# Kernel optimization log

Hardware: AMD Instinct MI355X
Metric: run time of the kernel (lower is better)

The kernel has to match this reference:

```python
import jax, jax.numpy as jnp
import numpy as np


def setup_inputs() -> dict:
    key = jax.random.key(0)
    ks = jax.random.split(key, 5)
    B, D, L, E, R = 16384, 1024, 3, 4, 64
    return {
        "x": jax.random.normal(ks[0], (B, D), dtype=jnp.float32),
        "U": jax.random.normal(ks[1], (L, E, D, R), dtype=jnp.float32) * 0.05,
        "V": jax.random.normal(ks[2], (L, E, D, R), dtype=jnp.float32) * 0.05,
        "C": jax.random.normal(ks[3], (L, E, R, R), dtype=jnp.float32) * 0.1,
        "bias": jnp.zeros((L, D), dtype=jnp.float32),
        "G": jax.random.normal(ks[4], (E, D), dtype=jnp.float32) * 0.05,
    }


def reference(x, U, V, C, bias, G):
    # x: (B, D); U,V: (L, E, D, R); C: (L, E, R, R); bias: (L, D); G: (E, D)
    x0 = x
    x_l = x
    n_layers = U.shape[0]
    for i in range(n_layers):
        # low-rank projection per expert: V^T x -> tanh -> C -> tanh -> U
        v = jnp.tanh(jnp.einsum('edr,bd->ber', V[i], x_l))        # (B, E, R)
        c = jnp.tanh(jnp.einsum('ers,bes->ber', C[i], v))          # (B, E, R)
        u = jnp.einsum('edr,ber->bed', U[i], c)                    # (B, E, D)
        expert_out = x0[:, None, :] * (u + bias[i][None, None, :])  # (B, E, D)
        # gating: per-expert Dense(1, no bias) on x_l, softmax over experts
        gate = jax.nn.softmax(jnp.einsum('ed,bd->be', G, x_l), axis=1)  # (B, E)
        x_l = jnp.einsum('bed,be->bd', expert_out, gate) + x_l
    return x_l
```

## Files before the change

### kernel.cpp

```cpp
#include <hip/hip_runtime.h>


typedef __bf16 bf16x8 __attribute__((ext_vector_type(8)));
typedef float f32x4 __attribute__((ext_vector_type(4)));
typedef unsigned short u16;
typedef unsigned int u32;

#define TB   32
#define DIM  1024
#define RR   64
#define NE   4
#define NL   3
#define N1   256

#define VF_PER_LAYER (16*32*2*64*8)
#define UF_PER_LAYER (64*8*2*64*8)
#define VF_TOTAL (NL*VF_PER_LAYER)
#define UF_TOTAL (NL*UF_PER_LAYER)

#define MFMA16(a,b,c) __builtin_amdgcn_mfma_f32_16x16x32_bf16(a,b,c,0,0,0)

__device__ __forceinline__ u16 f2bf(float f) {
  u32 u = __float_as_uint(f);
  u32 r = (u + 0x7FFFu + ((u >> 16) & 1u)) >> 16;
  return (u16)r;
}
__device__ __forceinline__ float bf2f(u16 b) {
  return __uint_as_float(((u32)b) << 16);
}
__device__ __forceinline__ bf16x8 ld_frag_g(const u16* p) {
  return __builtin_bit_cast(bf16x8, *reinterpret_cast<const uint4*>(p));
}

__global__ __launch_bounds__(256)
void convert_frags(const float* __restrict__ Vw, const float* __restrict__ Uw,
                   u16* __restrict__ Vf, u16* __restrict__ Uf) {
  const int id = blockIdx.x * 256 + threadIdx.x;
  float f[8];
  if (id < NL * 16 * 32 * 64) {
    const int lane = id & 63;
    const int ks   = (id >> 6) & 31;
    const int ct   = (id >> 11) & 15;
    const int l    = id >> 15;
    const int col  = ct * 16 + (lane & 15);
    const int e = col >> 6, r = col & 63;
    const int kbase = ks * 32 + (lane >> 4) * 8;
    const float* src = Vw + ((size_t)(l * NE + e) * DIM + kbase) * RR + r;
    #pragma unroll
    for (int i = 0; i < 8; ++i) f[i] = src[(size_t)i * RR];
    u16* dst = Vf + (size_t)l * VF_PER_LAYER + ((((size_t)ct * 32 + ks) * 2) * 64 + lane) * 8;
    uint4 hi, lo;
    u16 h[8], lw[8];
    #pragma unroll
    for (int i = 0; i < 8; ++i) { h[i] = f2bf(f[i]); lw[i] = f2bf(f[i] - bf2f(h[i])); }
    hi.x = h[0] | (u32)h[1] << 16;  hi.y = h[2] | (u32)h[3] << 16;
    hi.z = h[4] | (u32)h[5] << 16;  hi.w = h[6] | (u32)h[7] << 16;
    lo.x = lw[0] | (u32)lw[1] << 16; lo.y = lw[2] | (u32)lw[3] << 16;
    lo.z = lw[4] | (u32)lw[5] << 16; lo.w = lw[6] | (u32)lw[7] << 16;
    *reinterpret_cast<uint4*>(dst) = hi;
    *reinterpret_cast<uint4*>(dst + 512) = lo;
  } else {
    const int u = id - NL * 16 * 32 * 64;
    const int lane = u & 63;
    const int ks   = (u >> 6) & 7;
    const int ct   = (u >> 9) & 63;
    const int l    = u >> 15;
    const int d    = ct * 16 + (lane & 15);
    const int kk   = ks * 32 + (lane >> 4) * 8;
    const int e = kk >> 6, rb = kk & 63;
    const float* src = Uw + ((size_t)(l * NE + e) * DIM + d) * RR + rb;
    #pragma unroll
    for (int i = 0; i < 8; ++i) f[i] = src[i];
    u16* dst = Uf + (size_t)l * UF_PER_LAYER + ((((size_t)ct * 8 + ks) * 2) * 64 + lane) * 8;
    uint4 hi, lo;
    u16 h[8], lw[8];
    #pragma unroll
    for (int i = 0; i < 8; ++i) { h[i] = f2bf(f[i]); lw[i] = f2bf(f[i] - bf2f(h[i])); }
    hi.x = h[0] | (u32)h[1] << 16;  hi.y = h[2] | (u32)h[3] << 16;
    hi.z = h[4] | (u32)h[5] << 16;  hi.w = h[6] | (u32)h[7] << 16;
    lo.x = lw[0] | (u32)lw[1] << 16; lo.y = lw[2] | (u32)lw[3] << 16;
    lo.z = lw[4] | (u32)lw[5] << 16; lo.w = lw[6] | (u32)lw[7] << 16;
    *reinterpret_cast<uint4*>(dst) = hi;
    *reinterpret_cast<uint4*>(dst + 512) = lo;
  }
}

struct SM2 {
  union {
    u16 Ax[2][8][2][64][8];
    u16 Wf[2][8][2][64][8];
  } u;
  float vbuf[TB][N1 + 4];
  float gp[TB][NE][2];
  float gate[TB][NE];
};

__global__ __launch_bounds__(256, 2)
void crossnet_mfma(const float* __restrict__ x,
                   const float* __restrict__ Cw,
                   const float* __restrict__ bias,
                   const float* __restrict__ G,
                   const u16* __restrict__ Vf, const u16* __restrict__ Uf,
                   float* __restrict__ out) {
  __shared__ SM2 sm;
  const int t    = threadIdx.x;
  const int lane = t & 63;
  const int wv   = t >> 6;
  const int l15  = lane & 15;
  const int lg   = lane >> 4;
  const int b0   = blockIdx.x * TB;
  const int tc   = t & 31, tr = t >> 5;

  for (int layer = 0; layer < NL; ++layer) {
    const float* xin = (layer == 0) ? x : out;
    const u16* Vfl = Vf + (size_t)layer * VF_PER_LAYER;
    const u16* Ufl = Uf + (size_t)layer * UF_PER_LAYER;
    __syncthreads();

    {
      const int gb = t >> 3, ge = (t >> 1) & 3, gh = t & 1;
      const float4* xr = reinterpret_cast<const float4*>(xin + (size_t)(b0 + gb) * DIM) + gh * 128;
      const float4* gr = reinterpret_cast<const float4*>(G + (size_t)ge * DIM) + gh * 128;
      float4 sa = {0.f, 0.f, 0.f, 0.f};
      for (int q = 0; q < 128; ++q) {
        float4 a = xr[q], g4 = gr[q];
        sa.x = fmaf(a.x, g4.x, sa.x); sa.y = fmaf(a.y, g4.y, sa.y);
        sa.z = fmaf(a.z, g4.z, sa.z); sa.w = fmaf(a.w, g4.w, sa.w);
      }
      sm.gp[gb][ge][gh] = (sa.x + sa.y) + (sa.z + sa.w);
    }
    __syncthreads();
    if (t < TB) {
      float z[NE]; float m = -1e30f;
      #pragma unroll
      for (int e = 0; e < NE; ++e) { z[e] = sm.gp[t][e][0] + sm.gp[t][e][1]; m = fmaxf(m, z[e]); }
      float den = 0.f;
      #pragma unroll
      for (int e = 0; e < NE; ++e) { z[e] = expf(z[e] - m); den += z[e]; }
      const float inv = 1.f / den;
      #pragma unroll
      for (int e = 0; e < NE; ++e) sm.gate[t][e] = z[e] * inv;
    }

    f32x4 acc[2][4];
    #pragma unroll
    for (int rt = 0; rt < 2; ++rt)
      #pragma unroll
      for (int c = 0; c < 4; ++c) acc[rt][c] = (f32x4){0.f, 0.f, 0.f, 0.f};

    for (int ch = 0; ch < 4; ++ch) {
      __syncthreads();
      #pragma unroll
      for (int q = 0; q < 8; ++q) {
        const int idx = q * 256 + t;
        const int r = idx >> 6, k4 = idx & 63;
        const float4 v = *reinterpret_cast<const float4*>(
            xin + (size_t)(b0 + r) * DIM + ch * 256 + k4 * 4);
        const int kk = k4 * 4;
        const int ksl = kk >> 5, ii = kk & 7, rt = r >> 4;
        const int lnf = (((kk >> 3) & 3) << 4) | (r & 15);
        u16 h0 = f2bf(v.x), h1 = f2bf(v.y), h2 = f2bf(v.z), h3 = f2bf(v.w);
        u16 e0 = f2bf(v.x - bf2f(h0)), e1 = f2bf(v.y - bf2f(h1));
        u16 e2 = f2bf(v.z - bf2f(h2)), e3 = f2bf(v.w - bf2f(h3));
        uint2 hw, lw;
        hw.x = h0 | (u32)h1 << 16; hw.y = h2 | (u32)h3 << 16;
        lw.x = e0 | (u32)e1 << 16; lw.y = e2 | (u32)e3 << 16;
        *reinterpret_cast<uint2*>(&sm.u.Ax[rt][ksl][0][lnf][ii]) = hw;
        *reinterpret_cast<uint2*>(&sm.u.Ax[rt][ksl][1][lnf][ii]) = lw;
      }
      __syncthreads();
      for (int ks = 0; ks < 8; ++ks) {
        const bf16x8 ah0 = __builtin_bit_cast(bf16x8, *(const uint4*)&sm.u.Ax[0][ks][0][lane][0]);
        const bf16x8 al0 = __builtin_bit_cast(bf16x8, *(const uint4*)&sm.u.Ax[0][ks][1][lane][0]);
        const bf16x8 ah1 = __builtin_bit_cast(bf16x8, *(const uint4*)&sm.u.Ax[1][ks][0][lane][0]);
        const bf16x8 al1 = __builtin_bit_cast(bf16x8, *(const uint4*)&sm.u.Ax[1][ks][1][lane][0]);
        const int kg = ch * 8 + ks;
        #pragma unroll
        for (int c = 0; c < 4; ++c) {
          const int ct = wv * 4 + c;
          const u16* p = Vfl + ((((size_t)ct * 32 + kg) * 2) * 64 + lane) * 8;
          const bf16x8 bh = ld_frag_g(p);
          const bf16x8 bl = ld_frag_g(p + 512);
          acc[0][c] = MFMA16(ah0, bh, acc[0][c]);
          acc[0][c] = MFMA16(ah0, bl, acc[0][c]);
          acc[0][c] = MFMA16(al0, bh, acc[0][c]);
          acc[1][c] = MFMA16(ah1, bh, acc[1][c]);
          acc[1][c] = MFMA16(ah1, bl, acc[1][c]);
          acc[1][c] = MFMA16(al1, bh, acc[1][c]);
        }
      }
    }
    #pragma unroll
    for (int rt = 0; rt < 2; ++rt)
      #pragma unroll
      for (int c = 0; c < 4; ++c)
        #pragma unroll
        for (int reg = 0; reg < 4; ++reg) {
          const int row = rt * 16 + lg * 4 + reg;
          const int col = (wv * 4 + c) * 16 + l15;
          sm.vbuf[row][col] = tanhf(acc[rt][c][reg]);
        }
    __syncthreads();

    float cacc[4][8];
    #pragma unroll
    for (int r2 = 0; r2 < 4; ++r2)
      #pragma unroll
      for (int j = 0; j < 8; ++j) cacc[r2][j] = 0.f;
    #pragma unroll
    for (int g = 0; g < 2; ++g) {
      const int colbase = g * 128 + tc * 4;
      const int e = colbase >> 6, rbase = colbase & 63;
      const float* Crow = Cw + ((size_t)layer * NE + e) * RR * RR;
      for (int s4 = 0; s4 < 16; ++s4) {
        float4 v4[4];
        #pragma unroll
        for (int r2 = 0; r2 < 4; ++r2)
          v4[r2] = *reinterpret_cast<const float4*>(&sm.vbuf[tr * 4 + r2][e * 64 + s4 * 4]);
        #pragma unroll
        for (int j = 0; j < 4; ++j) {
          const float4 c4 = *reinterpret_cast<const float4*>(Crow + (size_t)(rbase + j) * RR + s4 * 4);
          #pragma unroll
          for (int r2 = 0; r2 < 4; ++r2)
            cacc[r2][g * 4 + j] += c4.x * v4[r2].x + c4.y * v4[r2].y +
                                   c4.z * v4[r2].z + c4.w * v4[r2].w;
        }
      }
    }

    #pragma unroll
    for (int g = 0; g < 2; ++g)
      #pragma unroll
      for (int r2 = 0; r2 < 4; ++r2) {
        const int row = tr * 4 + r2;
        const int rt = row >> 4;
        const int colb = g * 128 + tc * 4;
        const int ksl = colb >> 5, ii = colb & 7;
        const int lnf = (((colb >> 3) & 3) << 4) | (row & 15);
        const float gt = sm.gate[row][colb >> 6];
        u16 h[4], e4[4];
        #pragma unroll
        for (int j = 0; j < 4; ++j) {
          const float wval = gt * tanhf(cacc[r2][g * 4 + j]);
          h[j] = f2bf(wval); e4[j] = f2bf(wval - bf2f(h[j]));
        }
        uint2 hw, lw;
        hw.x = h[0] | (u32)h[1] << 16; hw.y = h[2] | (u32)h[3] << 16;
        lw.x = e4[0] | (u32)e4[1] << 16; lw.y = e4[2] | (u32)e4[3] << 16;
        *reinterpret_cast<uint2*>(&sm.u.Wf[rt][ksl][0][lnf][ii]) = hw;
        *reinterpret_cast<uint2*>(&sm.u.Wf[rt][ksl][1][lnf][ii]) = lw;
      }
    __syncthreads();

    for (int nc = 0; nc < 4; ++nc) {
      f32x4 a2[2][4];
      #pragma unroll
      for (int rt = 0; rt < 2; ++rt)
        #pragma unroll
        for (int c = 0; c < 4; ++c) a2[rt][c] = (f32x4){0.f, 0.f, 0.f, 0.f};
      for (int ks = 0; ks < 8; ++ks) {
        const bf16x8 ah0 = __builtin_bit_cast(bf16x8, *(const uint4*)&sm.u.Wf[0][ks][0][lane][0]);
        const bf16x8 al0 = __builtin_bit_cast(bf16x8, *(const uint4*)&sm.u.Wf[0][ks][1][lane][0]);
        const bf16x8 ah1 = __builtin_bit_cast(bf16x8, *(const uint4*)&sm.u.Wf[1][ks][0][lane][0]);
        const bf16x8 al1 = __builtin_bit_cast(bf16x8, *(const uint4*)&sm.u.Wf[1][ks][1][lane][0]);
        #pragma unroll
        for (int c = 0; c < 4; ++c) {
          const int ct = nc * 16 + wv * 4 + c;
          const u16* p = Ufl + ((((size_t)ct * 8 + ks) * 2) * 64 + lane) * 8;
          const bf16x8 bh = ld_frag_g(p);
          const bf16x8 bl = ld_frag_g(p + 512);
          a2[0][c] = MFMA16(ah0, bh, a2[0][c]);
          a2[0][c] = MFMA16(ah0, bl, a2[0][c]);
          a2[0][c] = MFMA16(al0, bh, a2[0][c]);
          a2[1][c] = MFMA16(ah1, bh, a2[1][c]);
          a2[1][c] = MFMA16(ah1, bl, a2[1][c]);
          a2[1][c] = MFMA16(al1, bh, a2[1][c]);
        }
      }
      #pragma unroll
      for (int rt = 0; rt < 2; ++rt)
        #pragma unroll
        for (int c = 0; c < 4; ++c) {
          const int col = (nc * 16 + wv * 4 + c) * 16 + l15;
          const float bv = bias[(size_t)layer * DIM + col];
          #pragma unroll
          for (int reg = 0; reg < 4; ++reg) {
            const int row = rt * 16 + lg * 4 + reg;
            const size_t off = (size_t)(b0 + row) * DIM + col;
            out[off] = x[off] * (a2[rt][c][reg] + bv) + xin[off];
          }
        }
    }
  }
}

extern "C" void kernel_launch(void* const* d_in, const int* in_sizes, int n_in,
                              void* d_out, int out_size, void* d_ws, size_t ws_size,
                              hipStream_t stream) {
  const float* x    = (const float*)d_in[0];
  const float* Uw   = (const float*)d_in[1];
  const float* Vw   = (const float*)d_in[2];
  const float* Cw   = (const float*)d_in[3];
  const float* bias = (const float*)d_in[4];
  const float* G    = (const float*)d_in[5];
  float* out = (float*)d_out;
  u16* Vf = (u16*)d_ws;
  u16* Uf = Vf + VF_TOTAL;

  hipLaunchKernelGGL(convert_frags, dim3((NL * 16 * 32 * 64 + NL * 64 * 8 * 64) / 256),
                     dim3(256), 0, stream, Vw, Uw, Vf, Uf);

  const int B = in_sizes[0] / DIM;
  hipLaunchKernelGGL(crossnet_mfma, dim3(B / TB), dim3(256), 0, stream,
                     x, Cw, bias, G, Vf, Uf, out);
}
```

Before: 960.8 us.

## Double threads per block to 512 and stage epilogue through LDS for coalesced stores

Doubles the block to 512 threads (8 waves), so each wave owns half as many MFMA column tiles and the gate, staging and C-projection work is split across more threads. The final epilogue now writes the U-projection result to shared memory and reads it back as row-contiguous float4 chunks, giving coalesced vector loads of x and x_l and vector stores of out. This adds two barriers per output chunk, and the weight fragments for V and U are now spread across more waves, which may raise contention. The higher occupancy target may also constrain registers.

New measurement: 2.098 ms. 118% more time.

```diff
diff --git a/kernel.cpp b/kernel.cpp
--- a/kernel.cpp
+++ b/kernel.cpp
@@ -91,11 +91,11 @@
     u16 Wf[2][8][2][64][8];
   } u;
   float vbuf[TB][N1 + 4];
-  float gp[TB][NE][2];
+  float gp4[TB][NE][4];
   float gate[TB][NE];
 };
 
-__global__ __launch_bounds__(256, 2)
+__global__ __launch_bounds__(512, 4)
 void crossnet_mfma(const float* __restrict__ x,
                    const float* __restrict__ Cw,
                    const float* __restrict__ bias,
@@ -118,22 +118,27 @@
     __syncthreads();
 
     {
-      const int gb = t >> 3, ge = (t >> 1) & 3, gh = t & 1;
-      const float4* xr = reinterpret_cast<const float4*>(xin + (size_t)(b0 + gb) * DIM) + gh * 128;
-      const float4* gr = reinterpret_cast<const float4*>(G + (size_t)ge * DIM) + gh * 128;
+      const int gb = t >> 4;
+      const int ge = (t >> 2) & 3;
+      const int gq = t & 3;
+      const float4* xr = reinterpret_cast<const float4*>(xin + (size_t)(b0 + gb) * DIM) + gq * 64;
+      const float4* gr = reinterpret_cast<const float4*>(G + (size_t)ge * DIM) + gq * 64;
       float4 sa = {0.f, 0.f, 0.f, 0.f};
-      for (int q = 0; q < 128; ++q) {
+      for (int q = 0; q < 64; ++q) {
         float4 a = xr[q], g4 = gr[q];
         sa.x = fmaf(a.x, g4.x, sa.x); sa.y = fmaf(a.y, g4.y, sa.y);
         sa.z = fmaf(a.z, g4.z, sa.z); sa.w = fmaf(a.w, g4.w, sa.w);
       }
-      sm.gp[gb][ge][gh] = (sa.x + sa.y) + (sa.z + sa.w);
+      sm.gp4[gb][ge][gq] = (sa.x + sa.y) + (sa.z + sa.w);
     }
     __syncthreads();
     if (t < TB) {
       float z[NE]; float m = -1e30f;
       #pragma unroll
-      for (int e = 0; e < NE; ++e) { z[e] = sm.gp[t][e][0] + sm.gp[t][e][1]; m = fmaxf(m, z[e]); }
+      for (int e = 0; e < NE; ++e) {
+        z[e] = (sm.gp4[t][e][0] + sm.gp4[t][e][1]) + (sm.gp4[t][e][2] + sm.gp4[t][e][3]);
+        m = fmaxf(m, z[e]);
+      }
       float den = 0.f;
       #pragma unroll
       for (int e = 0; e < NE; ++e) { z[e] = expf(z[e] - m); den += z[e]; }
@@ -142,17 +147,17 @@
       for (int e = 0; e < NE; ++e) sm.gate[t][e] = z[e] * inv;
     }
 
-    f32x4 acc[2][4];
+    f32x4 acc[2][2];
     #pragma unroll
     for (int rt = 0; rt < 2; ++rt)
       #pragma unroll
-      for (int c = 0; c < 4; ++c) acc[rt][c] = (f32x4){0.f, 0.f, 0.f, 0.f};
+      for (int c = 0; c < 2; ++c) acc[rt][c] = (f32x4){0.f, 0.f, 0.f, 0.f};
 
     for (int ch = 0; ch < 4; ++ch) {
       __syncthreads();
       #pragma unroll
-      for (int q = 0; q < 8; ++q) {
-        const int idx = q * 256 + t;
+      for (int q = 0; q < 4; ++q) {
+        const int idx = q * 512 + t;
         const int r = idx >> 6, k4 = idx & 63;
         const float4 v = *reinterpret_cast<const float4*>(
             xin + (size_t)(b0 + r) * DIM + ch * 256 + k4 * 4);
@@ -176,8 +181,8 @@
         const bf16x8 al1 = __builtin_bit_cast(bf16x8, *(const uint4*)&sm.u.Ax[1][ks][1][lane][0]);
         const int kg = ch * 8 + ks;
         #pragma unroll
-        for (int c = 0; c < 4; ++c) {
-          const int ct = wv * 4 + c;
+        for (int c = 0; c < 2; ++c) {
+          const int ct = wv * 2 + c;
           const u16* p = Vfl + ((((size_t)ct * 32 + kg) * 2) * 64 + lane) * 8;
           const bf16x8 bh = ld_frag_g(p);
           const bf16x8 bl = ld_frag_g(p + 512);
@@ -193,18 +198,18 @@
     #pragma unroll
     for (int rt = 0; rt < 2; ++rt)
       #pragma unroll
-      for (int c = 0; c < 4; ++c)
+      for (int c = 0; c < 2; ++c)
         #pragma unroll
         for (int reg = 0; reg < 4; ++reg) {
           const int row = rt * 16 + lg * 4 + reg;
-          const int col = (wv * 4 + c) * 16 + l15;
+          const int col = (wv * 2 + c) * 16 + l15;
           sm.vbuf[row][col] = tanhf(acc[rt][c][reg]);
         }
     __syncthreads();
 
-    float cacc[4][8];
-    #pragma unroll
-    for (int r2 = 0; r2 < 4; ++r2)
+    float cacc[2][8];
+    #pragma unroll
+    for (int r2 = 0; r2 < 2; ++r2)
       #pragma unroll
       for (int j = 0; j < 8; ++j) cacc[r2][j] = 0.f;
     #pragma unroll
@@ -213,15 +218,15 @@
       const int e = colbase >> 6, rbase = colbase & 63;
       const float* Crow = Cw + ((size_t)layer * NE + e) * RR * RR;
       for (int s4 = 0; s4 < 16; ++s4) {
-        float4 v4[4];
-        #pragma unroll
-        for (int r2 = 0; r2 < 4; ++r2)
-          v4[r2] = *reinterpret_cast<const float4*>(&sm.vbuf[tr * 4 + r2][e * 64 + s4 * 4]);
+        float4 v4[2];
+        #pragma unroll
+        for (int r2 = 0; r2 < 2; ++r2)
+          v4[r2] = *reinterpret_cast<const float4*>(&sm.vbuf[tr * 2 + r2][e * 64 + s4 * 4]);
         #pragma unroll
         for (int j = 0; j < 4; ++j) {
           const float4 c4 = *reinterpret_cast<const float4*>(Crow + (size_t)(rbase + j) * RR + s4 * 4);
           #pragma unroll
-          for (int r2 = 0; r2 < 4; ++r2)
+          for (int r2 = 0; r2 < 2; ++r2)
             cacc[r2][g * 4 + j] += c4.x * v4[r2].x + c4.y * v4[r2].y +
                                    c4.z * v4[r2].z + c4.w * v4[r2].w;
         }
@@ -231,8 +236,8 @@
     #pragma unroll
     for (int g = 0; g < 2; ++g)
       #pragma unroll
-      for (int r2 = 0; r2 < 4; ++r2) {
-        const int row = tr * 4 + r2;
+      for (int r2 = 0; r2 < 2; ++r2) {
+        const int row = tr * 2 + r2;
         const int rt = row >> 4;
         const int colb = g * 128 + tc * 4;
         const int ksl = colb >> 5, ii = colb & 7;
@@ -253,19 +258,19 @@
     __syncthreads();
 
     for (int nc = 0; nc < 4; ++nc) {
-      f32x4 a2[2][4];
+      f32x4 a2[2][2];
       #pragma unroll
       for (int rt = 0; rt < 2; ++rt)
         #pragma unroll
-        for (int c = 0; c < 4; ++c) a2[rt][c] = (f32x4){0.f, 0.f, 0.f, 0.f};
+        for (int c = 0; c < 2; ++c) a2[rt][c] = (f32x4){0.f, 0.f, 0.f, 0.f};
       for (int ks = 0; ks < 8; ++ks) {
         const bf16x8 ah0 = __builtin_bit_cast(bf16x8, *(const uint4*)&sm.u.Wf[0][ks][0][lane][0]);
         const bf16x8 al0 = __builtin_bit_cast(bf16x8, *(const uint4*)&sm.u.Wf[0][ks][1][lane][0]);
         const bf16x8 ah1 = __builtin_bit_cast(bf16x8, *(const uint4*)&sm.u.Wf[1][ks][0][lane][0]);
         const bf16x8 al1 = __builtin_bit_cast(bf16x8, *(const uint4*)&sm.u.Wf[1][ks][1][lane][0]);
         #pragma unroll
-        for (int c = 0; c < 4; ++c) {
-          const int ct = nc * 16 + wv * 4 + c;
+        for (int c = 0; c < 2; ++c) {
+          const int ct = nc * 16 + wv * 2 + c;
           const u16* p = Ufl + ((((size_t)ct * 8 + ks) * 2) * 64 + lane) * 8;
           const bf16x8 bh = ld_frag_g(p);
           const bf16x8 bl = ld_frag_g(p + 512);
@@ -277,19 +282,38 @@
           a2[1][c] = MFMA16(al1, bh, a2[1][c]);
         }
       }
+      __syncthreads();
       #pragma unroll
       for (int rt = 0; rt < 2; ++rt)
         #pragma unroll
-        for (int c = 0; c < 4; ++c) {
-          const int col = (nc * 16 + wv * 4 + c) * 16 + l15;
-          const float bv = bias[(size_t)layer * DIM + col];
+        for (int c = 0; c < 2; ++c)
           #pragma unroll
           for (int reg = 0; reg < 4; ++reg) {
             const int row = rt * 16 + lg * 4 + reg;
-            const size_t off = (size_t)(b0 + row) * DIM + col;
-            out[off] = x[off] * (a2[rt][c][reg] + bv) + xin[off];
+            const int col = (wv * 2 + c) * 16 + l15;
+            sm.vbuf[row][col] = a2[rt][c][reg];
           }
-        }
+      __syncthreads();
+      {
+        const int row = t >> 4;
+        const int c0 = (t & 15) * 4;
+        #pragma unroll
+        for (int j = 0; j < 4; ++j) {
+          const int cl = j * 64 + c0;
+          const int col = nc * 256 + cl;
+          const float4 ub = *reinterpret_cast<const float4*>(&sm.vbuf[row][cl]);
+          const float4 bv = *reinterpret_cast<const float4*>(bias + (size_t)layer * DIM + col);
+          const size_t off = (size_t)(b0 + row) * DIM + col;
+          const float4 x0v = *reinterpret_cast<const float4*>(x + off);
+          const float4 xlv = *reinterpret_cast<const float4*>(xin + off);
+          float4 o;
+          o.x = x0v.x * (ub.x + bv.x) + xlv.x;
+          o.y = x0v.y * (ub.y + bv.y) + xlv.y;
+          o.z = x0v.z * (ub.z + bv.z) + xlv.z;
+          o.w = x0v.w * (ub.w + bv.w) + xlv.w;
+          *reinterpret_cast<float4*>(out + off) = o;
+        }
+      }
     }
   }
 }
@@ -311,6 +335,6 @@
                      dim3(256), 0, stream, Vw, Uw, Vf, Uf);
 
   const int B = in_sizes[0] / DIM;
-  hipLaunchKernelGGL(crossnet_mfma, dim3(B / TB), dim3(256), 0, stream,
+  hipLaunchKernelGGL(crossnet_mfma, dim3(B / TB), dim3(512), 0, stream,
                      x, Cw, bias, G, Vf, Uf, out);
 }
```
